# Performance work log

Hardware: AMD Instinct MI355X
Metric: run time of the kernel (lower is better)

## Reference

```python
import jax, jax.numpy as jnp
import numpy as np

H = 12          # num attention heads
D = 768         # hidden size
DH = D // H     # head dim = 64

def setup_inputs() -> dict:
    key = jax.random.key(0)
    ks = jax.random.split(key, 9)
    B, N = 8, 1024
    s = 0.02
    return {
        "hidden_states": jax.random.normal(ks[0], (B, N, D), jnp.float32),
        "Wq": jax.random.normal(ks[1], (D, D), jnp.float32) * s,
        "bq": jnp.zeros((D,), jnp.float32),
        "Wk": jax.random.normal(ks[2], (D, D), jnp.float32) * s,
        "bk": jnp.zeros((D,), jnp.float32),
        "Wv": jax.random.normal(ks[3], (D, D), jnp.float32) * s,
        "bv": jnp.zeros((D,), jnp.float32),
        "Wo": jax.random.normal(ks[4], (D, D), jnp.float32) * s,
        "bo": jnp.zeros((D,), jnp.float32),
    }

def _split_heads(x):
    # [B, N, D] -> [B, H, N, DH]
    B, N, _ = x.shape
    return x.reshape(B, N, H, DH).transpose(0, 2, 1, 3)

def reference(hidden_states, Wq, bq, Wk, bk, Wv, bv, Wo, bo):
    # torch Linear: y = x @ W.T + b
    q = _split_heads(hidden_states @ Wq.T + bq)
    k = _split_heads(hidden_states @ Wk.T + bk)
    v = _split_heads(hidden_states @ Wv.T + bv)
    scale = 1.0 / jnp.sqrt(jnp.asarray(DH, hidden_states.dtype))
    scores = jnp.einsum("bhqd,bhkd->bhqk", q, k) * scale
    probs = jax.nn.softmax(scores, axis=-1)
    ctx = jnp.einsum("bhqk,bhkd->bhqd", probs, v)
    B, _, N, _ = ctx.shape
    ctx = ctx.transpose(0, 2, 1, 3).reshape(B, N, D)
    return ctx @ Wo.T + bo
```

## Files before the change

### kernel.cpp

```cpp
#include <hip/hip_runtime.h>

typedef unsigned short u16;
typedef unsigned int   u32;
typedef unsigned long long u64;
typedef __attribute__((ext_vector_type(8))) short bf16x8;
typedef __attribute__((ext_vector_type(4))) float f32x4;
typedef __attribute__((address_space(3))) u32 lds_u32;
typedef __attribute__((address_space(1))) u32 gbl_u32;

#define MFMA16(a,b,c) __builtin_amdgcn_mfma_f32_16x16x32_bf16((a),(b),(c),0,0,0)
#define QSCALE 0.1803368801111204f

#define WAIT3 do{ asm volatile("s_waitcnt vmcnt(3)" ::: "memory"); }while(0)
#define WAIT2 do{ asm volatile("s_waitcnt vmcnt(2)" ::: "memory"); }while(0)
#define WAIT0 do{ asm volatile("s_waitcnt vmcnt(0)" ::: "memory"); }while(0)
#define SCHED __builtin_amdgcn_sched_barrier(0)
#define BARR  __builtin_amdgcn_s_barrier()

__device__ __forceinline__ u16 f2bf(float f){
  u32 u = __builtin_bit_cast(u32, f);
  u32 r = u + 0x7fffu + ((u>>16)&1u);
  return (u16)(r>>16);
}
__device__ __forceinline__ float bf2f(u16 h){
  return __builtin_bit_cast(float, (u32)h<<16);
}

union V8 { u16 s[8]; uint4 v; };

__global__ __launch_bounds__(256) void cvt_all(const float* __restrict__ hs,
    const float* __restrict__ Wq, const float* __restrict__ Wk,
    const float* __restrict__ Wv, const float* __restrict__ Wo,
    u16* __restrict__ hsb, u16* __restrict__ wqkv, u16* __restrict__ woh)
{
  const int bid = blockIdx.x;
  if (bid < 3072){
    int i = bid*256 + threadIdx.x;
    const float4* p = (const float4*)(hs + (size_t)i*8);
    float4 a = p[0], b = p[1];
    V8 t;
    t.s[0]=f2bf(a.x); t.s[1]=f2bf(a.y); t.s[2]=f2bf(a.z); t.s[3]=f2bf(a.w);
    t.s[4]=f2bf(b.x); t.s[5]=f2bf(b.y); t.s[6]=f2bf(b.z); t.s[7]=f2bf(b.w);
    *(uint4*)(hsb + (size_t)i*8) = t.v;
    return;
  }
  const int r = bid - 3072;
  const int seg = r / 288;
  const int off = (r - seg*288)*256 + threadIdx.x;
  const float* src = seg==0?Wq: seg==1?Wk: seg==2?Wv: Wo;
  const float4* p = (const float4*)(src + (size_t)off*8);
  float4 a = p[0], b = p[1];
  float xs[8] = {a.x,a.y,a.z,a.w,b.x,b.y,b.z,b.w};
  V8 t;
  #pragma unroll
  for (int j=0;j<8;++j) t.s[j]=f2bf(xs[j]);
  if (seg < 3) *(uint4*)(wqkv + (size_t)seg*589824 + (size_t)off*8) = t.v;
  else         *(uint4*)(woh  + (size_t)off*8) = t.v;
}

__global__ __launch_bounds__(512) void mm_qkv(const u16* __restrict__ A, const u16* __restrict__ Bp,
    const float* __restrict__ bq, const float* __restrict__ bk, const float* __restrict__ bvv,
    u16* __restrict__ Oq, u16* __restrict__ Ok, u16* __restrict__ Ov)
{
  __shared__ u16 P[3][10240];
  const int bid = blockIdx.x;
  const int sid = (bid & 7)*96 + (bid >> 3);
  const int mb = sid/12, nb = sid - mb*12;
  const int m0 = mb*128, n0 = nb*192;
  const int tid = threadIdx.x;
  const int lane = tid&63, wid = tid>>6;
  const int wm = wid>>2, wn = wid&3;
  const int fr = lane&15, fg = lane>>4;

  const char* Ab = (const char*)A;
  const char* Bb = (const char*)Bp;
  const char* sp[3];
  int ldst[3];
  #pragma unroll
  for (int c=0;c<3;++c){
    int ci = c*512 + tid;
    if (c==2) ci = 1024 + tid;
    if (ci < 512){
      int line = ci>>3, slot = ci&7;
      int d = slot ^ (line&7);
      int row = 2*line + (d>>2);
      sp[c] = Ab + (size_t)(m0+row)*1536 + (d&3)*16;
    } else if (ci < 1280){
      int i = ci - 512;
      int line = i>>3, slot = i&7;
      int d = slot ^ (line&7);
      int row = 2*line + (d>>2);
      sp[c] = Bb + (size_t)(n0+row)*1536 + (d&3)*16;
    } else {
      sp[c] = Ab;
    }
    ldst[c] = ci*16;
  }

  const int sl = (((fr&1)<<2) + fg) ^ (fr>>1);
  const int aoff = (fr&~1)*64 + sl*16 + wm*4096;
  const int boff = 8192 + (fr&~1)*64 + sl*16 + wn*3072;

  f32x4 zz = {0.f,0.f,0.f,0.f};
  f32x4 acc[4][3];
  #pragma unroll
  for (int i=0;i<4;++i)
    #pragma unroll
    for (int j=0;j<3;++j) acc[i][j]=zz;

  auto STAGE = [&](int t, int b){
    char* dst0 = (char*)P[b];
    #pragma unroll
    for (int c=0;c<3;++c){
      if (c==2 && wid>=4) break;
      __builtin_amdgcn_global_load_lds((const gbl_u32*)(sp[c] + (size_t)t*64),
        (lds_u32*)(dst0 + ldst[c]), 16, 0, 0);
    }
  };
  auto COMPUTE = [&](int b){
    const char* pb = (const char*)P[b];
    bf16x8 bfr[3];
    #pragma unroll
    for (int nt=0;nt<3;++nt)
      bfr[nt] = *(const bf16x8*)(pb + boff + nt*1024);
    #pragma unroll
    for (int mt=0;mt<4;++mt){
      bf16x8 af = *(const bf16x8*)(pb + aoff + mt*1024);
      #pragma unroll
      for (int nt=0;nt<3;++nt)
        acc[mt][nt] = MFMA16(af, bfr[nt], acc[mt][nt]);
    }
  };

  STAGE(0, 0); STAGE(1, 1);
  int cb = 0;
  for (int t=0; t<24; ++t){
    if (t < 23){ if (wid < 4) WAIT3; else WAIT2; } else WAIT0;
    BARR; SCHED;
    if (t < 22){
      int sb = cb + 2; if (sb >= 3) sb -= 3;
      STAGE(t+2, sb);
    }
    __builtin_amdgcn_s_setprio(1);
    COMPUTE(cb);
    __builtin_amdgcn_s_setprio(0);
    cb = (cb == 2) ? 0 : cb + 1;
  }

  const int seg = nb/4;
  const float* bias = seg==0?bq: seg==1?bk:bvv;
  const float sc = (seg==0) ? QSCALE : 1.0f;
  if (seg < 2){
    u16* O = seg==0?Oq:Ok;
    #pragma unroll
    for (int mt=0;mt<4;++mt){
      #pragma unroll
      for (int nt=0;nt<3;++nt){
        int colw = n0 + wn*48 + nt*16 + fr - seg*768;
        float bz = bias[colw];
        int hh = colw>>6, d = colw&63;
        #pragma unroll
        for (int rr=0;rr<4;++rr){
          int row = m0 + wm*64 + mt*16 + fg*4 + rr;
          int b = row>>10, nn = row&1023;
          O[((size_t)(b*12+hh)<<16) + (size_t)nn*64 + d] = f2bf((acc[mt][nt][rr] + bz) * sc);
        }
      }
    }
  } else {
    #pragma unroll
    for (int mt=0;mt<4;++mt){
      #pragma unroll
      for (int nt=0;nt<3;++nt){
        int colw = n0 + wn*48 + nt*16 + fr - 1536;
        float bz = bias[colw];
        int hh = colw>>6, d = colw&63;
        int row0 = m0 + wm*64 + mt*16 + fg*4;
        int b = row0>>10, nn = row0&1023;
        union { u16 h[4]; u64 q; } pk;
        #pragma unroll
        for (int rr=0;rr<4;++rr) pk.h[rr] = f2bf(acc[mt][nt][rr] + bz);
        *(u64*)&Ov[((size_t)(b*12+hh)<<16) + (size_t)d*1024 + nn] = pk.q;
      }
    }
  }
}

__global__ __launch_bounds__(512) void mm_o(const u16* __restrict__ A, const u16* __restrict__ Bp,
                                            const float* __restrict__ bias, float* __restrict__ O)
{
  __shared__ u16 P[3][10240];
  const int bid = blockIdx.x;
  const int sid = (bid & 7)*32 + (bid >> 3);
  const int mb = sid/4, nb = sid & 3;
  const int m0 = mb*128, n0 = nb*192;
  const int tid = threadIdx.x;
  const int lane = tid&63, wid = tid>>6;
  const int wm = wid>>2, wn = wid&3;
  const int fr = lane&15, fg = lane>>4;

  const char* Ab = (const char*)A;
  const char* Bb = (const char*)Bp;
  const char* sp[3];
  int ldst[3];
  #pragma unroll
  for (int c=0;c<3;++c){
    int ci = c*512 + tid;
    if (c==2) ci = 1024 + tid;
    if (ci < 512){
      int line = ci>>3, slot = ci&7;
      int d = slot ^ (line&7);
      int row = 2*line + (d>>2);
      sp[c] = Ab + (size_t)(m0+row)*1536 + (d&3)*16;
    } else if (ci < 1280){
      int i = ci - 512;
      int line = i>>3, slot = i&7;
      int d = slot ^ (line&7);
      int row = 2*line + (d>>2);
      sp[c] = Bb + (size_t)(n0+row)*1536 + (d&3)*16;
    } else {
      sp[c] = Ab;
    }
    ldst[c] = ci*16;
  }

  const int sl = (((fr&1)<<2) + fg) ^ (fr>>1);
  const int aoff = (fr&~1)*64 + sl*16 + wm*4096;
  const int boff = 8192 + (fr&~1)*64 + sl*16 + wn*3072;

  f32x4 zz = {0.f,0.f,0.f,0.f};
  f32x4 acc[4][3];
  #pragma unroll
  for (int i=0;i<4;++i)
    #pragma unroll
    for (int j=0;j<3;++j) acc[i][j]=zz;

  auto STAGE = [&](int t, int b){
    char* dst0 = (char*)P[b];
    #pragma unroll
    for (int c=0;c<3;++c){
      if (c==2 && wid>=4) break;
      __builtin_amdgcn_global_load_lds((const gbl_u32*)(sp[c] + (size_t)t*64),
        (lds_u32*)(dst0 + ldst[c]), 16, 0, 0);
    }
  };
  auto COMPUTE = [&](int b){
    const char* pb = (const char*)P[b];
    bf16x8 bfr[3];
    #pragma unroll
    for (int nt=0;nt<3;++nt)
      bfr[nt] = *(const bf16x8*)(pb + boff + nt*1024);
    #pragma unroll
    for (int mt=0;mt<4;++mt){
      bf16x8 af = *(const bf16x8*)(pb + aoff + mt*1024);
      #pragma unroll
      for (int nt=0;nt<3;++nt)
        acc[mt][nt] = MFMA16(af, bfr[nt], acc[mt][nt]);
    }
  };

  STAGE(0, 0); STAGE(1, 1);
  int cb = 0;
  for (int t=0; t<24; ++t){
    if (t < 23){ if (wid < 4) WAIT3; else WAIT2; } else WAIT0;
    BARR; SCHED;
    if (t < 22){
      int sb = cb + 2; if (sb >= 3) sb -= 3;
      STAGE(t+2, sb);
    }
    __builtin_amdgcn_s_setprio(1);
    COMPUTE(cb);
    __builtin_amdgcn_s_setprio(0);
    cb = (cb == 2) ? 0 : cb + 1;
  }

  #pragma unroll
  for (int mt=0;mt<4;++mt){
    #pragma unroll
    for (int nt=0;nt<3;++nt){
      int colb = n0 + wn*48 + nt*16 + fr;
      float bz = bias[colb];
      #pragma unroll
      for (int rr=0;rr<4;++rr){
        int row = m0 + wm*64 + mt*16 + fg*4 + rr;
        O[(size_t)row*768 + colb] = acc[mt][nt][rr] + bz;
      }
    }
  }
}

__global__ __launch_bounds__(256) void attn(const u16* __restrict__ qh, const u16* __restrict__ kh,
                                            const u16* __restrict__ vh, u16* __restrict__ ch)
{
  __shared__ u16 Kb[2][4096];
  __shared__ u16 Vb[2][4096];
  __shared__ u16 Ps[4][32][72];
  const int tid=threadIdx.x, w=tid>>6, lane=tid&63;
  const int fr=lane&15, fg=lane>>4;
  const int bh=blockIdx.x, qt=blockIdx.y;
  const size_t base=(size_t)bh<<16;
  const int q0=qt*128 + w*32;

  const char* kbase = (const char*)(kh + base);
  const char* vbase = (const char*)(vh + base);

  int koff[2], voff[2];
  #pragma unroll
  for (int c=0;c<2;++c){
    int ci = c*256 + tid;
    int row = ci>>3;
    int colp = ((ci&7)*16) ^ ((row&7)<<4);
    koff[c] = row*128  + colp;
    voff[c] = row*2048 + colp;
  }

  bf16x8 qf[2][2];
  #pragma unroll
  for (int mt=0;mt<2;++mt)
    #pragma unroll
    for (int ks=0;ks<2;++ks)
      qf[mt][ks] = *(const bf16x8*)&qh[base + (size_t)(q0+mt*16+fr)*64 + ks*32 + fg*8];

  const int swz = (fr&7)<<4;
  int lowD[2];
  #pragma unroll
  for (int ks=0;ks<2;++ks) lowD[ks] = (ks*64 + fg*16) ^ swz;
  const int frbase = fr*128;

  const short one_bf = (short)0x3F80;
  bf16x8 ones = {one_bf,one_bf,one_bf,one_bf,one_bf,one_bf,one_bf,one_bf};

  f32x4 zz = {0.f,0.f,0.f,0.f};
  f32x4 o[2][4];
  f32x4 ol[2];
  #pragma unroll
  for (int mt=0;mt<2;++mt){
    ol[mt]=zz;
    #pragma unroll
    for (int j=0;j<4;++j) o[mt][j]=zz;
  }

  {
    #pragma unroll
    for (int c=0;c<2;++c){
      __builtin_amdgcn_global_load_lds((const gbl_u32*)(kbase + koff[c]),
        (lds_u32*)((char*)&Kb[0][0] + c*4096 + w*1024), 16, 0, 0);
      __builtin_amdgcn_global_load_lds((const gbl_u32*)(vbase + voff[c]),
        (lds_u32*)((char*)&Vb[0][0] + c*4096 + w*1024), 16, 0, 0);
    }
  }
  __syncthreads();

  for (int kt=0; kt<16; ++kt){
    const int buf = kt & 1;
    {
      const int ktn = (kt+1) & 15;
      const char* kt_ = kbase + ktn*8192;
      const char* vt_ = vbase + ktn*128;
      #pragma unroll
      for (int c=0;c<2;++c){
        __builtin_amdgcn_global_load_lds((const gbl_u32*)(kt_ + koff[c]),
          (lds_u32*)((char*)&Kb[buf^1][0] + c*4096 + w*1024), 16, 0, 0);
        __builtin_amdgcn_global_load_lds((const gbl_u32*)(vt_ + voff[c]),
          (lds_u32*)((char*)&Vb[buf^1][0] + c*4096 + w*1024), 16, 0, 0);
      }
    }

    f32x4 s[2][4];
    #pragma unroll
    for (int mt=0;mt<2;++mt)
      #pragma unroll
      for (int j=0;j<4;++j) s[mt][j]=zz;
    const char* kb = (const char*)&Kb[buf][0];
    __builtin_amdgcn_s_setprio(1);
    #pragma unroll
    for (int ct=0;ct<4;++ct){
      #pragma unroll
      for (int ks=0;ks<2;++ks){
        bf16x8 kf = *(const bf16x8*)(kb + ct*2048 + frbase + lowD[ks]);
        s[0][ct]=MFMA16(kf,qf[0][ks],s[0][ct]);
        s[1][ct]=MFMA16(kf,qf[1][ks],s[1][ct]);
      }
    }
    __builtin_amdgcn_s_setprio(0);

    #pragma unroll
    for (int mt=0;mt<2;++mt){
      #pragma unroll
      for (int ct=0;ct<4;++ct){
        float e0 = __builtin_amdgcn_exp2f(s[mt][ct][0]);
        float e1 = __builtin_amdgcn_exp2f(s[mt][ct][1]);
        float e2 = __builtin_amdgcn_exp2f(s[mt][ct][2]);
        float e3 = __builtin_amdgcn_exp2f(s[mt][ct][3]);
        u32 w0, w1;
        asm("v_cvt_pk_bf16_f32 %0, %1, %2" : "=v"(w0) : "v"(e0), "v"(e1));
        asm("v_cvt_pk_bf16_f32 %0, %1, %2" : "=v"(w1) : "v"(e2), "v"(e3));
        uint2 pk2; pk2.x = w0; pk2.y = w1;
        *(uint2*)&Ps[w][mt*16+fr][ct*16+fg*4] = pk2;
      }
    }

    const char* vb = (const char*)&Vb[buf][0];
    __builtin_amdgcn_s_setprio(1);
    #pragma unroll
    for (int ks2=0;ks2<2;++ks2){
      bf16x8 vf[4];
      #pragma unroll
      for (int dt=0;dt<4;++dt)
        vf[dt] = *(const bf16x8*)(vb + dt*2048 + frbase + lowD[ks2]);
      #pragma unroll
      for (int mt=0;mt<2;++mt){
        bf16x8 pa = *(const bf16x8*)&Ps[w][mt*16+fr][ks2*32+fg*8];
        #pragma unroll
        for (int dt=0;dt<4;++dt)
          o[mt][dt]=MFMA16(pa, vf[dt], o[mt][dt]);
        ol[mt]=MFMA16(pa, ones, ol[mt]);
      }
    }
    __builtin_amdgcn_s_setprio(0);

    __syncthreads();
  }

  const int b=bh/12, hd=bh%12;
  #pragma unroll
  for (int mt=0;mt<2;++mt){
    float inv[4];
    #pragma unroll
    for (int rr=0;rr<4;++rr) inv[rr] = 1.0f / ol[mt][rr];
    #pragma unroll
    for (int dt=0;dt<4;++dt){
      int d = dt*16 + fr;
      #pragma unroll
      for (int rr=0;rr<4;++rr){
        int n = q0 + mt*16 + fg*4 + rr;
        ch[((size_t)b*1024 + n)*768 + hd*64 + d] = f2bf(o[mt][dt][rr] * inv[rr]);
      }
    }
  }
}

extern "C" void kernel_launch(void* const* d_in, const int* in_sizes, int n_in,
                              void* d_out, int out_size, void* d_ws, size_t ws_size,
                              hipStream_t stream) {
  const float* hs = (const float*)d_in[0];
  const float* Wq = (const float*)d_in[1];
  const float* bq = (const float*)d_in[2];
  const float* Wk = (const float*)d_in[3];
  const float* bk = (const float*)d_in[4];
  const float* Wv = (const float*)d_in[5];
  const float* bv = (const float*)d_in[6];
  const float* Wo = (const float*)d_in[7];
  const float* bo = (const float*)d_in[8];
  float* out = (float*)d_out;

  const size_t PS = (size_t)8192*768;
  u16* ws16  = (u16*)d_ws;
  u16* hs_bf = ws16;
  u16* q_bf  = ws16 + PS;
  u16* k_bf  = ws16 + 2*PS;
  u16* v_bf  = ws16 + 3*PS;
  u16* wqkv  = ws16 + 4*PS;
  u16* woh   = wqkv + 3*589824;
  u16* c_hi  = hs_bf;

  dim3 blk(256);
  cvt_all<<<3072 + 4*288, blk, 0, stream>>>(hs, Wq, Wk, Wv, Wo, hs_bf, wqkv, woh);
  mm_qkv<<<768, dim3(512), 0, stream>>>(hs_bf, wqkv, bq, bk, bv, q_bf, k_bf, v_bf);
  attn<<<dim3(96,8), blk, 0, stream>>>(q_bf, k_bf, v_bf, c_hi);
  mm_o<<<256, dim3(512), 0, stream>>>(c_hi, woh, bo, out);
}
```

Measured before the change: 106.7 us.

## Use 32x32x16 MFMA in attention and keep probabilities in registers via permlane swap

Switches the attention kernel from 16x16x32 MFMA tiles to 32x32x16 tiles for both the QK^T and PV products. The probability matrix now goes directly from the score accumulators into A-operand fragments using v_permlane32_swap, so the per-wave LDS P buffer and its write/read round trip are removed. Launch bounds now request 3 blocks per CU. This cuts LDS traffic and instruction count per tile, but changes the register layout and swizzle addressing, which must still match the K/V LDS layout.

Result: faster. 104.4 us (median of 2 runs) (-2.2%).

```diff
diff --git a/kernel.cpp b/kernel.cpp
--- a/kernel.cpp
+++ b/kernel.cpp
@@ -5,10 +5,12 @@
 typedef unsigned long long u64;
 typedef __attribute__((ext_vector_type(8))) short bf16x8;
 typedef __attribute__((ext_vector_type(4))) float f32x4;
+typedef __attribute__((ext_vector_type(16))) float f32x16;
 typedef __attribute__((address_space(3))) u32 lds_u32;
 typedef __attribute__((address_space(1))) u32 gbl_u32;
 
 #define MFMA16(a,b,c) __builtin_amdgcn_mfma_f32_16x16x32_bf16((a),(b),(c),0,0,0)
+#define MFMA32(a,b,c) __builtin_amdgcn_mfma_f32_32x32x16_bf16((a),(b),(c),0,0,0)
 #define QSCALE 0.1803368801111204f
 
 #define WAIT3 do{ asm volatile("s_waitcnt vmcnt(3)" ::: "memory"); }while(0)
@@ -289,14 +291,13 @@
   }
 }
 
-__global__ __launch_bounds__(256) void attn(const u16* __restrict__ qh, const u16* __restrict__ kh,
-                                            const u16* __restrict__ vh, u16* __restrict__ ch)
+__global__ __launch_bounds__(256, 3) void attn(const u16* __restrict__ qh, const u16* __restrict__ kh,
+                                               const u16* __restrict__ vh, u16* __restrict__ ch)
 {
   __shared__ u16 Kb[2][4096];
   __shared__ u16 Vb[2][4096];
-  __shared__ u16 Ps[4][32][72];
   const int tid=threadIdx.x, w=tid>>6, lane=tid&63;
-  const int fr=lane&15, fg=lane>>4;
+  const int l31 = lane&31, h = lane>>5;
   const int bh=blockIdx.x, qt=blockIdx.y;
   const size_t base=(size_t)bh<<16;
   const int q0=qt*128 + w*32;
@@ -314,31 +315,20 @@
     voff[c] = row*2048 + colp;
   }
 
-  bf16x8 qf[2][2];
-  #pragma unroll
-  for (int mt=0;mt<2;++mt)
-    #pragma unroll
-    for (int ks=0;ks<2;++ks)
-      qf[mt][ks] = *(const bf16x8*)&qh[base + (size_t)(q0+mt*16+fr)*64 + ks*32 + fg*8];
-
-  const int swz = (fr&7)<<4;
-  int lowD[2];
-  #pragma unroll
-  for (int ks=0;ks<2;++ks) lowD[ks] = (ks*64 + fg*16) ^ swz;
-  const int frbase = fr*128;
+  bf16x8 qf[4];
+  #pragma unroll
+  for (int ks=0;ks<4;++ks)
+    qf[ks] = *(const bf16x8*)&qh[base + (size_t)(q0+l31)*64 + ks*16 + h*8];
+
+  const int swz3 = (lane&7)<<4;
+  const int dbase = (h<<4) ^ swz3;
+  const int krow = l31*128;
 
   const short one_bf = (short)0x3F80;
   bf16x8 ones = {one_bf,one_bf,one_bf,one_bf,one_bf,one_bf,one_bf,one_bf};
 
-  f32x4 zz = {0.f,0.f,0.f,0.f};
-  f32x4 o[2][4];
-  f32x4 ol[2];
-  #pragma unroll
-  for (int mt=0;mt<2;++mt){
-    ol[mt]=zz;
-    #pragma unroll
-    for (int j=0;j<4;++j) o[mt][j]=zz;
-  }
+  f32x16 z16 = {0.f,0.f,0.f,0.f,0.f,0.f,0.f,0.f,0.f,0.f,0.f,0.f,0.f,0.f,0.f,0.f};
+  f32x16 o0 = z16, o1 = z16, ol = z16;
 
   {
     #pragma unroll
@@ -366,55 +356,58 @@
       }
     }
 
-    f32x4 s[2][4];
-    #pragma unroll
-    for (int mt=0;mt<2;++mt)
-      #pragma unroll
-      for (int j=0;j<4;++j) s[mt][j]=zz;
-    const char* kb = (const char*)&Kb[buf][0];
+    const char* kb_ = (const char*)&Kb[buf][0];
+    f32x16 s0 = z16, s1 = z16;
     __builtin_amdgcn_s_setprio(1);
     #pragma unroll
-    for (int ct=0;ct<4;++ct){
-      #pragma unroll
-      for (int ks=0;ks<2;++ks){
-        bf16x8 kf = *(const bf16x8*)(kb + ct*2048 + frbase + lowD[ks]);
-        s[0][ct]=MFMA16(kf,qf[0][ks],s[0][ct]);
-        s[1][ct]=MFMA16(kf,qf[1][ks],s[1][ct]);
-      }
+    for (int ks=0;ks<4;++ks){
+      int db = dbase ^ (ks<<5);
+      bf16x8 kf0 = *(const bf16x8*)(kb_ + krow + db);
+      bf16x8 kf1 = *(const bf16x8*)(kb_ + 4096 + krow + db);
+      s0 = MFMA32(kf0, qf[ks], s0);
+      s1 = MFMA32(kf1, qf[ks], s1);
     }
     __builtin_amdgcn_s_setprio(0);
 
-    #pragma unroll
-    for (int mt=0;mt<2;++mt){
-      #pragma unroll
-      for (int ct=0;ct<4;++ct){
-        float e0 = __builtin_amdgcn_exp2f(s[mt][ct][0]);
-        float e1 = __builtin_amdgcn_exp2f(s[mt][ct][1]);
-        float e2 = __builtin_amdgcn_exp2f(s[mt][ct][2]);
-        float e3 = __builtin_amdgcn_exp2f(s[mt][ct][3]);
-        u32 w0, w1;
-        asm("v_cvt_pk_bf16_f32 %0, %1, %2" : "=v"(w0) : "v"(e0), "v"(e1));
-        asm("v_cvt_pk_bf16_f32 %0, %1, %2" : "=v"(w1) : "v"(e2), "v"(e3));
-        uint2 pk2; pk2.x = w0; pk2.y = w1;
-        *(uint2*)&Ps[w][mt*16+fr][ct*16+fg*4] = pk2;
-      }
-    }
-
-    const char* vb = (const char*)&Vb[buf][0];
+    bf16x8 paf[2][2];
+    #pragma unroll
+    for (int kbi=0;kbi<2;++kbi){
+      const f32x16& sb = kbi ? s1 : s0;
+      #pragma unroll
+      for (int kp=0;kp<2;++kp){
+        float e0 = __builtin_amdgcn_exp2f(sb[kp*8+0]);
+        float e1 = __builtin_amdgcn_exp2f(sb[kp*8+1]);
+        float e2 = __builtin_amdgcn_exp2f(sb[kp*8+2]);
+        float e3 = __builtin_amdgcn_exp2f(sb[kp*8+3]);
+        float e4 = __builtin_amdgcn_exp2f(sb[kp*8+4]);
+        float e5 = __builtin_amdgcn_exp2f(sb[kp*8+5]);
+        float e6 = __builtin_amdgcn_exp2f(sb[kp*8+6]);
+        float e7 = __builtin_amdgcn_exp2f(sb[kp*8+7]);
+        u32 x, y, uu, vv;
+        asm("v_cvt_pk_bf16_f32 %0, %1, %2" : "=v"(x)  : "v"(e0), "v"(e1));
+        asm("v_cvt_pk_bf16_f32 %0, %1, %2" : "=v"(y)  : "v"(e2), "v"(e3));
+        asm("v_cvt_pk_bf16_f32 %0, %1, %2" : "=v"(uu) : "v"(e4), "v"(e5));
+        asm("v_cvt_pk_bf16_f32 %0, %1, %2" : "=v"(vv) : "v"(e6), "v"(e7));
+        asm volatile("v_permlane32_swap_b32 %0, %1" : "+v"(x), "+v"(uu));
+        asm volatile("v_permlane32_swap_b32 %0, %1" : "+v"(y), "+v"(vv));
+        union { u32 u[4]; bf16x8 v; } fx;
+        fx.u[0]=x; fx.u[1]=y; fx.u[2]=uu; fx.u[3]=vv;
+        paf[kbi][kp] = fx.v;
+      }
+    }
+
+    const char* vb_ = (const char*)&Vb[buf][0];
     __builtin_amdgcn_s_setprio(1);
     #pragma unroll
-    for (int ks2=0;ks2<2;++ks2){
-      bf16x8 vf[4];
-      #pragma unroll
-      for (int dt=0;dt<4;++dt)
-        vf[dt] = *(const bf16x8*)(vb + dt*2048 + frbase + lowD[ks2]);
-      #pragma unroll
-      for (int mt=0;mt<2;++mt){
-        bf16x8 pa = *(const bf16x8*)&Ps[w][mt*16+fr][ks2*32+fg*8];
-        #pragma unroll
-        for (int dt=0;dt<4;++dt)
-          o[mt][dt]=MFMA16(pa, vf[dt], o[mt][dt]);
-        ol[mt]=MFMA16(pa, ones, ol[mt]);
+    for (int kbi=0;kbi<2;++kbi){
+      #pragma unroll
+      for (int kp=0;kp<2;++kp){
+        int vcol = dbase ^ (kp<<5) ^ (kbi<<6);
+        bf16x8 vf0 = *(const bf16x8*)(vb_ + l31*128 + vcol);
+        bf16x8 vf1 = *(const bf16x8*)(vb_ + (32+l31)*128 + vcol);
+        o0 = MFMA32(paf[kbi][kp], vf0, o0);
+        o1 = MFMA32(paf[kbi][kp], vf1, o1);
+        ol = MFMA32(paf[kbi][kp], ones, ol);
       }
     }
     __builtin_amdgcn_s_setprio(0);
@@ -423,19 +416,17 @@
   }
 
   const int b=bh/12, hd=bh%12;
-  #pragma unroll
-  for (int mt=0;mt<2;++mt){
-    float inv[4];
-    #pragma unroll
-    for (int rr=0;rr<4;++rr) inv[rr] = 1.0f / ol[mt][rr];
-    #pragma unroll
-    for (int dt=0;dt<4;++dt){
-      int d = dt*16 + fr;
-      #pragma unroll
-      for (int rr=0;rr<4;++rr){
-        int n = q0 + mt*16 + fg*4 + rr;
-        ch[((size_t)b*1024 + n)*768 + hd*64 + d] = f2bf(o[mt][dt][rr] * inv[rr]);
-      }
+  float inv[16];
+  #pragma unroll
+  for (int rg=0;rg<16;++rg) inv[rg] = 1.0f / ol[rg];
+  #pragma unroll
+  for (int nt=0;nt<2;++nt){
+    #pragma unroll
+    for (int rg=0;rg<16;++rg){
+      int q = q0 + (rg&3) + 8*(rg>>2) + 4*h;
+      int d = nt*32 + l31;
+      float val = (nt ? o1[rg] : o0[rg]) * inv[rg];
+      ch[((size_t)b*1024 + q)*768 + hd*64 + d] = f2bf(val);
     }
   }
 }
```
